# Kernel tuning notes

Measured on AMD Instinct MI355X. Metric: run time of the kernel, lower is better.

The kernel has to match this reference:

```python
import jax, jax.numpy as jnp
import numpy as np

B, S, D, H = 4, 1024, 1024, 16
HD = D // H  # head dim = 64


def setup_inputs() -> dict:
    key = jax.random.key(0)
    ks = jax.random.split(key, 7)
    return {
        "x": jax.random.normal(ks[0], (B, S, D), dtype=jnp.float32),
        "w_attn": jax.random.normal(ks[1], (D, 3 * D), dtype=jnp.float32) * 0.02,
        "b_attn": jax.random.normal(ks[2], (3 * D,), dtype=jnp.float32) * 0.02,
        "w_proj": jax.random.normal(ks[3], (D, D), dtype=jnp.float32) * 0.02,
        "b_proj": jax.random.normal(ks[4], (D,), dtype=jnp.float32) * 0.02,
        "attn_override": jax.random.uniform(ks[5], (H, S, S), dtype=jnp.float32),
        "attn_override_mask": jax.random.randint(ks[6], (H, S, S), 0, 2).astype(bool),
    }


def reference(x, w_attn, b_attn, w_proj, b_proj, attn_override, attn_override_mask):
    # c_attn (GPT-2 Conv1D): x @ W + b, then split into q, k, v
    qkv = jnp.einsum("bsd,de->bse", x, w_attn) + b_attn
    q, k, v = jnp.split(qkv, 3, axis=-1)
    # split heads: q,v -> [B,H,S,hd]; k -> [B,H,hd,S]
    q = q.reshape(B, S, H, HD).transpose(0, 2, 1, 3)
    k = k.reshape(B, S, H, HD).transpose(0, 2, 3, 1)
    v = v.reshape(B, S, H, HD).transpose(0, 2, 1, 3)
    # present buffer: stack(key.transpose(-2,-1), value) -> [2,B,H,S,hd]
    present = jnp.stack((k.transpose(0, 1, 3, 2), v))
    # scores with scaling
    w = jnp.einsum("bhqd,bhdk->bhqk", q, k) / jnp.sqrt(jnp.asarray(HD, x.dtype))
    # GPT-2 causal bias: w*b - 10000*(1-b)
    b = jnp.tril(jnp.ones((S, S), dtype=x.dtype))[None, None]
    w = w * b - 10000.0 * (1.0 - b)
    w = jax.nn.softmax(w, axis=-1)
    # attn_dropout: identity (eval). Override attention weights (broadcast over batch).
    w = jnp.where(attn_override_mask[None], attn_override[None], w)
    a = jnp.einsum("bhqk,bhkd->bhqd", w, v)
    # merge heads -> [B,S,D], then c_proj; resid_dropout identity (eval)
    a = a.transpose(0, 2, 1, 3).reshape(B, S, D)
    a = jnp.einsum("bsd,de->bse", a, w_proj) + b_proj
    return a, present
```

## Files before the change

kernel.cpp:

```cpp
#include <hip/hip_runtime.h>
#include <hip/hip_bf16.h>

#define Bdim 4
#define Sdim 1024
#define Ddim 1024
#define Hdim 16
#define HDdim 64

typedef __attribute__((ext_vector_type(8))) short short8;
typedef __attribute__((ext_vector_type(4))) float f32x4;
typedef __attribute__((ext_vector_type(2))) unsigned int uint2v;
typedef __attribute__((ext_vector_type(4))) unsigned short ushort4v;

#define AS1 __attribute__((address_space(1)))
#define AS3 __attribute__((address_space(3)))

__device__ __forceinline__ unsigned short f2bf(float x) {
    unsigned int u = __builtin_bit_cast(unsigned int, x);
    return (unsigned short)((u + 0x7fffu + ((u >> 16) & 1u)) >> 16);
}
__device__ __forceinline__ float bf2f(unsigned short u) {
    unsigned int v = ((unsigned int)u) << 16;
    return __builtin_bit_cast(float, v);
}

__global__ __launch_bounds__(256) void conv_bf16(const float* __restrict__ in,
                                                 unsigned short* __restrict__ out) {
    int i = blockIdx.x * 256 + threadIdx.x;
    float4 v = ((const float4*)in)[i];
    uint2v p;
    p.x = (unsigned)f2bf(v.x) | ((unsigned)f2bf(v.y) << 16);
    p.y = (unsigned)f2bf(v.z) | ((unsigned)f2bf(v.w) << 16);
    ((uint2v*)out)[i] = p;
}

__global__ __launch_bounds__(256) void transpose_bf16(const float* __restrict__ W,
                                                      unsigned short* __restrict__ Wt,
                                                      int K, int N) {
    __shared__ float t[32][33];
    const int tk = blockIdx.y * 32, tn = blockIdx.x * 32;
    const int r = threadIdx.x >> 5, c = threadIdx.x & 31;
    #pragma unroll
    for (int j = 0; j < 4; j++)
        t[r + 8 * j][c] = W[(size_t)(tk + r + 8 * j) * N + tn + c];
    __syncthreads();
    #pragma unroll
    for (int j = 0; j < 4; j++) {
        int nn = r + 8 * j;
        Wt[(size_t)(tn + nn) * K + tk + c] = f2bf(t[c][nn]);
    }
}

__global__ __launch_bounds__(256) void ovr_prep(const float* __restrict__ ovr,
                                                const int* __restrict__ msk,
                                                unsigned short* __restrict__ ovrb,
                                                unsigned long long* __restrict__ mbits) {
    size_t i = (size_t)blockIdx.x * 256 + threadIdx.x;
    ovrb[i] = f2bf(ovr[i]);
    unsigned long long bal = __ballot(msk[i] != 0);
    if ((threadIdx.x & 63) == 0) mbits[i >> 6] = bal;
}

__global__ __launch_bounds__(256) void kv_prep(const float* __restrict__ kout,
                                               const float* __restrict__ vout,
                                               unsigned short* __restrict__ Kb,
                                               unsigned short* __restrict__ Vtr) {
    const int bh = blockIdx.y;
    const int s0 = blockIdx.x * 64;
    const int tid = threadIdx.x;
    __shared__ float t[64][65];
    const float4* kbase = (const float4*)(kout + ((size_t)bh * Sdim + s0) * HDdim);
    const float4* vbase = (const float4*)(vout + ((size_t)bh * Sdim + s0) * HDdim);
    uint2v* kb = (uint2v*)(Kb + ((size_t)bh * Sdim + s0) * HDdim);
    #pragma unroll
    for (int i = 0; i < 4; i++) {
        int idx = tid + i * 256;
        float4 v = kbase[idx];
        uint2v p;
        p.x = (unsigned)f2bf(v.x) | ((unsigned)f2bf(v.y) << 16);
        p.y = (unsigned)f2bf(v.z) | ((unsigned)f2bf(v.w) << 16);
        kb[idx] = p;
        float4 vv = vbase[idx];
        int r = idx >> 4, c = (idx & 15) * 4;
        t[r][c + 0] = vv.x; t[r][c + 1] = vv.y; t[r][c + 2] = vv.z; t[r][c + 3] = vv.w;
    }
    __syncthreads();
    #pragma unroll
    for (int i = 0; i < 4; i++) {
        int idx = tid + i * 256;
        int d = idx >> 4, sc = (idx & 15) * 4;
        uint2v p;
        p.x = (unsigned)f2bf(t[sc + 0][d]) | ((unsigned)f2bf(t[sc + 1][d]) << 16);
        p.y = (unsigned)f2bf(t[sc + 2][d]) | ((unsigned)f2bf(t[sc + 3][d]) << 16);
        *(uint2v*)(Vtr + (size_t)bh * HDdim * Sdim + (size_t)d * Sdim + s0 + sc) = p;
    }
}

#define GEMM_BODY(Aptr, Bptr)                                                          \
    __shared__ unsigned short As[128 * 32];                                            \
    __shared__ unsigned short Bs[128 * 32];                                            \
    const int tid = threadIdx.x;                                                       \
    const int lane = tid & 63, w = tid >> 6;                                           \
    const int wm = w >> 1, wn = w & 1;                                                 \
    const int l15 = lane & 15, lg = lane >> 4;                                         \
    const int tile_m = blockIdx.y * 128, tile_n = blockIdx.x * 128;                    \
    f32x4 acc[4][4] = {};                                                              \
    for (int k0 = 0; k0 < 1024; k0 += 32) {                                            \
        _Pragma("unroll")                                                              \
        for (int j = 0; j < 2; j++) {                                                  \
            int ca = j * 256 + tid;                                                    \
            int rowa = ca >> 2, offa = (ca & 3) * 16;                                  \
            const char* ga = (const char*)(Aptr) +                                     \
                ((size_t)(tile_m + rowa) * 1024 + k0) * 2 + offa;                      \
            char* la = (char*)As + (j * 256 + w * 64) * 16;                            \
            __builtin_amdgcn_global_load_lds((const AS1 void*)ga, (AS3 void*)la,       \
                                             16, 0, 0);                                \
            const char* gb = (const char*)(Bptr) +                                     \
                ((size_t)(tile_n + rowa) * 1024 + k0) * 2 + offa;                      \
            char* lb = (char*)Bs + (j * 256 + w * 64) * 16;                            \
            __builtin_amdgcn_global_load_lds((const AS1 void*)gb, (AS3 void*)lb,       \
                                             16, 0, 0);                                \
        }                                                                              \
        __syncthreads();                                                               \
        short8 af[4], bfr[4];                                                          \
        _Pragma("unroll")                                                              \
        for (int t4 = 0; t4 < 4; t4++) {                                               \
            af[t4] = *(const short8*)((const char*)As +                                \
                        (wm * 64 + t4 * 16 + l15) * 64 + lg * 16);                     \
            bfr[t4] = *(const short8*)((const char*)Bs +                               \
                        (wn * 64 + t4 * 16 + l15) * 64 + lg * 16);                     \
        }                                                                              \
        _Pragma("unroll")                                                              \
        for (int i = 0; i < 4; i++)                                                    \
            _Pragma("unroll")                                                          \
            for (int j2 = 0; j2 < 4; j2++)                                             \
                acc[i][j2] = __builtin_amdgcn_mfma_f32_16x16x32_bf16(                  \
                    af[i], bfr[j2], acc[i][j2], 0, 0, 0);                              \
        __syncthreads();                                                               \
    }

__global__ __launch_bounds__(256) void gemm_qkv_mfma(const unsigned short* __restrict__ Xb,
                                                     const unsigned short* __restrict__ Wt,
                                                     const float* __restrict__ bias,
                                                     unsigned short* __restrict__ qbuf,
                                                     float* __restrict__ kout,
                                                     float* __restrict__ vout) {
    GEMM_BODY(Xb, Wt)
    const int seg = tile_n >> 10;
    #pragma unroll
    for (int i = 0; i < 4; i++) {
        #pragma unroll
        for (int j2 = 0; j2 < 4; j2++) {
            int n = tile_n + wn * 64 + j2 * 16 + l15;
            float bv = bias[n];
            int nn = n & 1023, h = nn >> 6, d = nn & 63;
            #pragma unroll
            for (int r = 0; r < 4; r++) {
                int m = tile_m + wm * 64 + i * 16 + 4 * lg + r;
                float v = acc[i][j2][r] + bv;
                int bb = m >> 10, s = m & 1023;
                size_t oidx = ((size_t)((bb * Hdim + h) * Sdim + s)) * HDdim + d;
                if (seg == 0) qbuf[oidx] = f2bf(v * 0.125f);
                else if (seg == 1) kout[oidx] = v;
                else vout[oidx] = v;
            }
        }
    }
}

__global__ __launch_bounds__(256) void gemm_proj_mfma(const unsigned short* __restrict__ Ab,
                                                      const unsigned short* __restrict__ Wt,
                                                      const float* __restrict__ bias,
                                                      float* __restrict__ out) {
    GEMM_BODY(Ab, Wt)
    #pragma unroll
    for (int i = 0; i < 4; i++) {
        #pragma unroll
        for (int j2 = 0; j2 < 4; j2++) {
            int n = tile_n + wn * 64 + j2 * 16 + l15;
            float bv = bias[n];
            #pragma unroll
            for (int r = 0; r < 4; r++) {
                int m = tile_m + wm * 64 + i * 16 + 4 * lg + r;
                out[(size_t)m * Ddim + n] = acc[i][j2][r] + bv;
            }
        }
    }
}

__global__ __launch_bounds__(256) void attn_mfma2(const unsigned short* __restrict__ qbuf,
                                                  const unsigned short* __restrict__ Kb,
                                                  const unsigned short* __restrict__ Vtr,
                                                  const unsigned short* __restrict__ ovrb,
                                                  const unsigned long long* __restrict__ mbits,
                                                  unsigned short* __restrict__ abuf) {
    const int qt = blockIdx.x;
    const int bh = blockIdx.y;
    const int h = bh & (Hdim - 1);
    const int b = bh >> 4;
    const int tid = threadIdx.x;
    const int wq = tid >> 6;
    const int lane = tid & 63;
    const int l15 = lane & 15;
    const int lg = lane >> 4;

    __shared__ unsigned short Ps[4][16 * 64];

    const unsigned short* kb = Kb + (size_t)bh * Sdim * HDdim;
    const unsigned short* vt = Vtr + (size_t)bh * HDdim * Sdim;
    const int qrow = qt * 64 + wq * 16 + l15;

    short8 qf[2];
    {
        const unsigned short* qr = qbuf + ((size_t)bh * Sdim + qrow) * HDdim;
        qf[0] = *(const short8*)(qr + 8 * lg);
        qf[1] = *(const short8*)(qr + 8 * lg + 32);
    }

    float m_run = -1e30f, l_run = 0.f;
    for (int kt = 0; kt <= qt; kt++) {
        float sv[16];
        const bool diag = (kt == qt);
        #pragma unroll
        for (int ks = 0; ks < 4; ks++) {
            const unsigned short* krow = kb + (size_t)(kt * 64 + ks * 16 + l15) * HDdim;
            short8 a0 = *(const short8*)(krow + 8 * lg);
            short8 a1 = *(const short8*)(krow + 8 * lg + 32);
            f32x4 c = {0.f, 0.f, 0.f, 0.f};
            c = __builtin_amdgcn_mfma_f32_16x16x32_bf16(a0, qf[0], c, 0, 0, 0);
            c = __builtin_amdgcn_mfma_f32_16x16x32_bf16(a1, qf[1], c, 0, 0, 0);
            #pragma unroll
            for (int r = 0; r < 4; r++) {
                int kg = kt * 64 + ks * 16 + 4 * lg + r;
                float s = c[r];
                if (diag && kg > qrow) s = -1e30f;
                sv[ks * 4 + r] = s;
            }
        }
        float tm = -1e30f;
        #pragma unroll
        for (int i = 0; i < 16; i++) tm = fmaxf(tm, sv[i]);
        tm = fmaxf(tm, __shfl_xor(tm, 16));
        tm = fmaxf(tm, __shfl_xor(tm, 32));
        float mn = fmaxf(m_run, tm);
        float ts = 0.f;
        #pragma unroll
        for (int i = 0; i < 16; i++) ts += __expf(sv[i] - mn);
        ts += __shfl_xor(ts, 16);
        ts += __shfl_xor(ts, 32);
        l_run = l_run * __expf(m_run - mn) + ts;
        m_run = mn;
    }
    const float inv_l = 1.f / l_run;

    f32x4 acc[4];
    #pragma unroll
    for (int ds = 0; ds < 4; ds++) acc[ds] = (f32x4){0.f, 0.f, 0.f, 0.f};
    const unsigned short* ob_base = ovrb + ((size_t)h * Sdim + qrow) * Sdim;
    const unsigned long long* mb_base = mbits + ((size_t)h * Sdim + qrow) * (Sdim / 64);

    for (int kt = 0; kt < 16; kt++) {
        float w[16];
        if (kt <= qt) {
            const bool diag = (kt == qt);
            #pragma unroll
            for (int ks = 0; ks < 4; ks++) {
                const unsigned short* krow = kb + (size_t)(kt * 64 + ks * 16 + l15) * HDdim;
                short8 a0 = *(const short8*)(krow + 8 * lg);
                short8 a1 = *(const short8*)(krow + 8 * lg + 32);
                f32x4 c = {0.f, 0.f, 0.f, 0.f};
                c = __builtin_amdgcn_mfma_f32_16x16x32_bf16(a0, qf[0], c, 0, 0, 0);
                c = __builtin_amdgcn_mfma_f32_16x16x32_bf16(a1, qf[1], c, 0, 0, 0);
                #pragma unroll
                for (int r = 0; r < 4; r++) {
                    int kg = kt * 64 + ks * 16 + 4 * lg + r;
                    float p = __expf(c[r] - m_run) * inv_l;
                    if (diag && kg > qrow) p = 0.f;
                    w[ks * 4 + r] = p;
                }
            }
        } else {
            #pragma unroll
            for (int i = 0; i < 16; i++) w[i] = 0.f;
        }
        unsigned long long mw = mb_base[kt];
        #pragma unroll
        for (int ks = 0; ks < 4; ks++) {
            int kb0 = kt * 64 + ks * 16 + 4 * lg;
            ushort4v o4 = *(const ushort4v*)(ob_base + kb0);
            int bit0 = ks * 16 + 4 * lg;
            #pragma unroll
            for (int r = 0; r < 4; r++)
                if ((mw >> (bit0 + r)) & 1ULL) w[ks * 4 + r] = bf2f(o4[r]);
        }
        #pragma unroll
        for (int ks = 0; ks < 4; ks++) {
            uint2v p;
            p.x = (unsigned)f2bf(w[ks * 4 + 0]) | ((unsigned)f2bf(w[ks * 4 + 1]) << 16);
            p.y = (unsigned)f2bf(w[ks * 4 + 2]) | ((unsigned)f2bf(w[ks * 4 + 3]) << 16);
            int byte = l15 * 128 + (ks * 16 + 4 * lg) * 2;
            byte ^= (l15 & 7) << 4;
            *(uint2v*)((char*)(Ps[wq]) + byte) = p;
        }
        int pbyte0 = l15 * 128 + lg * 16;
        pbyte0 ^= (l15 & 7) << 4;
        short8 pa0 = *(const short8*)((const char*)(Ps[wq]) + pbyte0);
        short8 pa1 = *(const short8*)((const char*)(Ps[wq]) + (pbyte0 ^ 64));
        #pragma unroll
        for (int ds = 0; ds < 4; ds++) {
            const unsigned short* vrow = vt + (size_t)(ds * 16 + l15) * Sdim + kt * 64;
            short8 v0 = *(const short8*)(vrow + 8 * lg);
            short8 v1 = *(const short8*)(vrow + 8 * lg + 32);
            acc[ds] = __builtin_amdgcn_mfma_f32_16x16x32_bf16(pa0, v0, acc[ds], 0, 0, 0);
            acc[ds] = __builtin_amdgcn_mfma_f32_16x16x32_bf16(pa1, v1, acc[ds], 0, 0, 0);
        }
    }

    #pragma unroll
    for (int ds = 0; ds < 4; ds++) {
        #pragma unroll
        for (int r = 0; r < 4; r++) {
            int q = qt * 64 + wq * 16 + 4 * lg + r;
            int d = h * HDdim + ds * 16 + l15;
            abuf[((size_t)(b * Sdim + q)) * Ddim + d] = f2bf(acc[ds][r]);
        }
    }
}

extern "C" void kernel_launch(void* const* d_in, const int* in_sizes, int n_in,
                              void* d_out, int out_size, void* d_ws, size_t ws_size,
                              hipStream_t stream) {
    const float* x       = (const float*)d_in[0];
    const float* w_attn  = (const float*)d_in[1];
    const float* b_attn  = (const float*)d_in[2];
    const float* w_proj  = (const float*)d_in[3];
    const float* b_proj  = (const float*)d_in[4];
    const float* ovr     = (const float*)d_in[5];
    const int*   msk     = (const int*)d_in[6];

    float* out = (float*)d_out;
    float* a_out = out;
    float* kout  = out + (size_t)Bdim * Sdim * Ddim;
    float* vout  = kout + (size_t)Bdim * Hdim * Sdim * HDdim;

    char* ws = (char*)d_ws;
    unsigned short* qbuf = (unsigned short*)ws;
    unsigned short* abuf = (unsigned short*)(ws + (8  << 20));
    unsigned short* Xb   = (unsigned short*)(ws + (16 << 20));
    unsigned short* Wta  = (unsigned short*)(ws + (24 << 20));
    unsigned short* Wtp  = (unsigned short*)(ws + (30 << 20));
    unsigned short* Kb   = (unsigned short*)(ws + (32 << 20));
    unsigned short* Vtr  = (unsigned short*)(ws + (40 << 20));
    unsigned short* ovrb = (unsigned short*)(ws + (48 << 20));
    unsigned long long* mbits = (unsigned long long*)(ws + (80 << 20));

    conv_bf16<<<dim3(4096), 256, 0, stream>>>(x, Xb);
    transpose_bf16<<<dim3(96, 32), 256, 0, stream>>>(w_attn, Wta, 1024, 3072);
    transpose_bf16<<<dim3(32, 32), 256, 0, stream>>>(w_proj, Wtp, 1024, 1024);
    ovr_prep<<<dim3(65536), 256, 0, stream>>>(ovr, msk, ovrb, mbits);

    gemm_qkv_mfma<<<dim3(24, 32), 256, 0, stream>>>(Xb, Wta, b_attn, qbuf, kout, vout);

    kv_prep<<<dim3(16, 64), 256, 0, stream>>>(kout, vout, Kb, Vtr);

    attn_mfma2<<<dim3(16, 64), 256, 0, stream>>>(qbuf, Kb, Vtr, ovrb, mbits, abuf);

    gemm_proj_mfma<<<dim3(8, 32), 256, 0, stream>>>(abuf, Wtp, b_proj, a_out);
}
```

Before: 471.8 us.

## Split override PV into dense GEMM and make causal attention single-pass flash

After: 483.7 us. 1.03x slower.

```diff
diff --git a/kernel.cpp b/kernel.cpp
--- a/kernel.cpp
+++ b/kernel.cpp
@@ -10,7 +10,6 @@
 typedef __attribute__((ext_vector_type(8))) short short8;
 typedef __attribute__((ext_vector_type(4))) float f32x4;
 typedef __attribute__((ext_vector_type(2))) unsigned int uint2v;
-typedef __attribute__((ext_vector_type(4))) unsigned short ushort4v;
 
 #define AS1 __attribute__((address_space(1)))
 #define AS3 __attribute__((address_space(3)))
@@ -53,11 +52,12 @@
 
 __global__ __launch_bounds__(256) void ovr_prep(const float* __restrict__ ovr,
                                                 const int* __restrict__ msk,
-                                                unsigned short* __restrict__ ovrb,
+                                                unsigned short* __restrict__ ovrm,
                                                 unsigned long long* __restrict__ mbits) {
     size_t i = (size_t)blockIdx.x * 256 + threadIdx.x;
-    ovrb[i] = f2bf(ovr[i]);
-    unsigned long long bal = __ballot(msk[i] != 0);
+    bool m = (msk[i] != 0);
+    ovrm[i] = m ? f2bf(ovr[i]) : (unsigned short)0;
+    unsigned long long bal = __ballot(m);
     if ((threadIdx.x & 63) == 0) mbits[i >> 6] = bal;
 }
 
@@ -188,11 +188,48 @@
     }
 }
 
-__global__ __launch_bounds__(256) void attn_mfma2(const unsigned short* __restrict__ qbuf,
+__global__ __launch_bounds__(256) void ovr_pv(const unsigned short* __restrict__ ovrm,
+                                              const unsigned short* __restrict__ Vtr,
+                                              unsigned short* __restrict__ obuf) {
+    const int qt = blockIdx.x;
+    const int bh = blockIdx.y;
+    const int h = bh & (Hdim - 1);
+    const int b = bh >> 4;
+    const int wq = threadIdx.x >> 6;
+    const int lane = threadIdx.x & 63;
+    const int l15 = lane & 15;
+    const int lg = lane >> 4;
+    const int qrow = qt * 64 + wq * 16 + l15;
+
+    const unsigned short* ob = ovrm + ((size_t)h * Sdim + qrow) * Sdim;
+    const unsigned short* vt = Vtr + (size_t)bh * HDdim * Sdim;
+
+    f32x4 acc[4] = {};
+    #pragma unroll 4
+    for (int kc = 0; kc < 32; kc++) {
+        short8 af = *(const short8*)(ob + kc * 32 + 8 * lg);
+        #pragma unroll
+        for (int ds = 0; ds < 4; ds++) {
+            short8 vf = *(const short8*)(vt + (size_t)(ds * 16 + l15) * Sdim + kc * 32 + 8 * lg);
+            acc[ds] = __builtin_amdgcn_mfma_f32_16x16x32_bf16(af, vf, acc[ds], 0, 0, 0);
+        }
+    }
+    #pragma unroll
+    for (int ds = 0; ds < 4; ds++) {
+        #pragma unroll
+        for (int r = 0; r < 4; r++) {
+            int q = qt * 64 + wq * 16 + 4 * lg + r;
+            int d = h * HDdim + ds * 16 + l15;
+            obuf[((size_t)(b * Sdim + q)) * Ddim + d] = f2bf(acc[ds][r]);
+        }
+    }
+}
+
+__global__ __launch_bounds__(256) void attn_flash(const unsigned short* __restrict__ qbuf,
                                                   const unsigned short* __restrict__ Kb,
                                                   const unsigned short* __restrict__ Vtr,
-                                                  const unsigned short* __restrict__ ovrb,
                                                   const unsigned long long* __restrict__ mbits,
+                                                  const unsigned short* __restrict__ obuf,
                                                   unsigned short* __restrict__ abuf) {
     const int qt = blockIdx.x;
     const int bh = blockIdx.y;
@@ -217,10 +254,16 @@
         qf[1] = *(const short8*)(qr + 8 * lg + 32);
     }
 
+    const unsigned long long* mb_base = mbits + ((size_t)h * Sdim + qrow) * (Sdim / 64);
+
     float m_run = -1e30f, l_run = 0.f;
+    f32x4 acc[4];
+    #pragma unroll
+    for (int ds = 0; ds < 4; ds++) acc[ds] = (f32x4){0.f, 0.f, 0.f, 0.f};
+
     for (int kt = 0; kt <= qt; kt++) {
+        const bool diag = (kt == qt);
         float sv[16];
-        const bool diag = (kt == qt);
         #pragma unroll
         for (int ks = 0; ks < 4; ks++) {
             const unsigned short* krow = kb + (size_t)(kt * 64 + ks * 16 + l15) * HDdim;
@@ -243,55 +286,33 @@
         tm = fmaxf(tm, __shfl_xor(tm, 16));
         tm = fmaxf(tm, __shfl_xor(tm, 32));
         float mn = fmaxf(m_run, tm);
+        float sc = __expf(m_run - mn);
         float ts = 0.f;
         #pragma unroll
         for (int i = 0; i < 16; i++) ts += __expf(sv[i] - mn);
         ts += __shfl_xor(ts, 16);
         ts += __shfl_xor(ts, 32);
-        l_run = l_run * __expf(m_run - mn) + ts;
+        l_run = l_run * sc + ts;
         m_run = mn;
-    }
-    const float inv_l = 1.f / l_run;
-
-    f32x4 acc[4];
-    #pragma unroll
-    for (int ds = 0; ds < 4; ds++) acc[ds] = (f32x4){0.f, 0.f, 0.f, 0.f};
-    const unsigned short* ob_base = ovrb + ((size_t)h * Sdim + qrow) * Sdim;
-    const unsigned long long* mb_base = mbits + ((size_t)h * Sdim + qrow) * (Sdim / 64);
-
-    for (int kt = 0; kt < 16; kt++) {
+        float sc0 = __shfl(sc, 4 * lg + 0);
+        float sc1 = __shfl(sc, 4 * lg + 1);
+        float sc2 = __shfl(sc, 4 * lg + 2);
+        float sc3 = __shfl(sc, 4 * lg + 3);
+        #pragma unroll
+        for (int ds = 0; ds < 4; ds++) {
+            acc[ds][0] *= sc0; acc[ds][1] *= sc1; acc[ds][2] *= sc2; acc[ds][3] *= sc3;
+        }
+        unsigned long long mw = mb_base[kt];
         float w[16];
-        if (kt <= qt) {
-            const bool diag = (kt == qt);
-            #pragma unroll
-            for (int ks = 0; ks < 4; ks++) {
-                const unsigned short* krow = kb + (size_t)(kt * 64 + ks * 16 + l15) * HDdim;
-                short8 a0 = *(const short8*)(krow + 8 * lg);
-                short8 a1 = *(const short8*)(krow + 8 * lg + 32);
-                f32x4 c = {0.f, 0.f, 0.f, 0.f};
-                c = __builtin_amdgcn_mfma_f32_16x16x32_bf16(a0, qf[0], c, 0, 0, 0);
-                c = __builtin_amdgcn_mfma_f32_16x16x32_bf16(a1, qf[1], c, 0, 0, 0);
-                #pragma unroll
-                for (int r = 0; r < 4; r++) {
-                    int kg = kt * 64 + ks * 16 + 4 * lg + r;
-                    float p = __expf(c[r] - m_run) * inv_l;
-                    if (diag && kg > qrow) p = 0.f;
-                    w[ks * 4 + r] = p;
-                }
-            }
-        } else {
-            #pragma unroll
-            for (int i = 0; i < 16; i++) w[i] = 0.f;
-        }
-        unsigned long long mw = mb_base[kt];
         #pragma unroll
         for (int ks = 0; ks < 4; ks++) {
-            int kb0 = kt * 64 + ks * 16 + 4 * lg;
-            ushort4v o4 = *(const ushort4v*)(ob_base + kb0);
             int bit0 = ks * 16 + 4 * lg;
             #pragma unroll
-            for (int r = 0; r < 4; r++)
-                if ((mw >> (bit0 + r)) & 1ULL) w[ks * 4 + r] = bf2f(o4[r]);
+            for (int r = 0; r < 4; r++) {
+                float p = __expf(sv[ks * 4 + r] - mn);
+                if ((mw >> (bit0 + r)) & 1ULL) p = 0.f;
+                w[ks * 4 + r] = p;
+            }
         }
         #pragma unroll
         for (int ks = 0; ks < 4; ks++) {
@@ -316,13 +337,21 @@
         }
     }
 
+    float inv_l = 1.f / l_run;
+    float i0 = __shfl(inv_l, 4 * lg + 0);
+    float i1 = __shfl(inv_l, 4 * lg + 1);
+    float i2 = __shfl(inv_l, 4 * lg + 2);
+    float i3 = __shfl(inv_l, 4 * lg + 3);
     #pragma unroll
     for (int ds = 0; ds < 4; ds++) {
+        f32x4 o = acc[ds];
+        o[0] *= i0; o[1] *= i1; o[2] *= i2; o[3] *= i3;
         #pragma unroll
         for (int r = 0; r < 4; r++) {
             int q = qt * 64 + wq * 16 + 4 * lg + r;
             int d = h * HDdim + ds * 16 + l15;
-            abuf[((size_t)(b * Sdim + q)) * Ddim + d] = f2bf(acc[ds][r]);
+            size_t idx = ((size_t)(b * Sdim + q)) * Ddim + d;
+            abuf[idx] = f2bf(o[r] + bf2f(obuf[idx]));
         }
     }
 }
@@ -347,23 +376,26 @@
     unsigned short* qbuf = (unsigned short*)ws;
     unsigned short* abuf = (unsigned short*)(ws + (8  << 20));
     unsigned short* Xb   = (unsigned short*)(ws + (16 << 20));
+    unsigned short* obuf = Xb;
     unsigned short* Wta  = (unsigned short*)(ws + (24 << 20));
     unsigned short* Wtp  = (unsigned short*)(ws + (30 << 20));
     unsigned short* Kb   = (unsigned short*)(ws + (32 << 20));
     unsigned short* Vtr  = (unsigned short*)(ws + (40 << 20));
-    unsigned short* ovrb = (unsigned short*)(ws + (48 << 20));
+    unsigned short* ovrm = (unsigned short*)(ws + (48 << 20));
     unsigned long long* mbits = (unsigned long long*)(ws + (80 << 20));
 
     conv_bf16<<<dim3(4096), 256, 0, stream>>>(x, Xb);
     transpose_bf16<<<dim3(96, 32), 256, 0, stream>>>(w_attn, Wta, 1024, 3072);
     transpose_bf16<<<dim3(32, 32), 256, 0, stream>>>(w_proj, Wtp, 1024, 1024);
-    ovr_prep<<<dim3(65536), 256, 0, stream>>>(ovr, msk, ovrb, mbits);
+    ovr_prep<<<dim3(65536), 256, 0, stream>>>(ovr, msk, ovrm, mbits);
 
     gemm_qkv_mfma<<<dim3(24, 32), 256, 0, stream>>>(Xb, Wta, b_attn, qbuf, kout, vout);
 
     kv_prep<<<dim3(16, 64), 256, 0, stream>>>(kout, vout, Kb, Vtr);
 
-    attn_mfma2<<<dim3(16, 64), 256, 0, stream>>>(qbuf, Kb, Vtr, ovrb, mbits, abuf);
+    ovr_pv<<<dim3(16, 64), 256, 0, stream>>>(ovrm, Vtr, obuf);
+
+    attn_flash<<<dim3(16, 64), 256, 0, stream>>>(qbuf, Kb, Vtr, mbits, obuf, abuf);
 
     gemm_proj_mfma<<<dim3(8, 32), 256, 0, stream>>>(abuf, Wtp, b_proj, a_out);
 }
```
